# Kernel optimization log

Hardware: AMD Instinct MI355X
Metric: run time of the kernel (lower is better)

## Reference

```python
import jax, jax.numpy as jnp
from jax import lax
import numpy as np

B, S, T = 1024, 512, 48


def setup_inputs() -> dict:
    key = jax.random.key(0)
    k1, k2, k3, k4, k5, k6 = jax.random.split(key, 6)
    emissions = jax.random.normal(k1, (B, S, T), dtype=jnp.float32)
    tags = jax.random.randint(k2, (B, S), 0, T, dtype=jnp.int32)
    # variable-length mask; length >= 1 so position 0 is always valid
    lengths = jax.random.randint(k3, (B,), 1, S + 1, dtype=jnp.int32)
    mask = (jnp.arange(S)[None, :] < lengths[:, None]).astype(jnp.float32)
    transitions = jax.random.normal(k4, (T, T), dtype=jnp.float32)
    start_transitions = jax.random.normal(k5, (T,), dtype=jnp.float32)
    end_transitions = jax.random.normal(k6, (T,), dtype=jnp.float32)
    return {
        "emissions": emissions,
        "tags": tags,
        "mask": mask,
        "transitions": transitions,
        "start_transitions": start_transitions,
        "end_transitions": end_transitions,
    }


def _gold_score(emissions, tags, mask, transitions, start_transitions, end_transitions):
    # score of the gold tag sequence (vectorized over time)
    score = start_transitions[tags[:, 0]]
    score = score + jnp.take_along_axis(emissions[:, 0], tags[:, 0:1], axis=1)[:, 0]
    # NOTE: original code indexes transitions[cur_tag, prev_tag] here (faithful)
    trans_sc = transitions[tags[:, 1:], tags[:, :-1]]                      # [B, S-1]
    emit_sc = jnp.take_along_axis(emissions[:, 1:], tags[:, 1:, None], axis=2)[..., 0]
    score = score + jnp.sum((trans_sc + emit_sc) * mask[:, 1:], axis=1)
    seq_last = mask.sum(axis=1).astype(jnp.int32) - 1                      # [B]
    last_tags = jnp.take_along_axis(tags, seq_last[:, None], axis=1)[:, 0]
    return score + end_transitions[last_tags]


def _forward_algorithm(emissions, mask, transitions, start_transitions, end_transitions):
    # log-partition via logsumexp recurrence, lax.scan over time
    init = start_transitions[None, :] + emissions[:, 0]                    # [B, T]

    def step(score, xs):
        em_i, m_i = xs                                                     # [B,T], [B]
        # next[b, cur] = logsumexp_prev(score[b,prev] + trans[prev,cur] + em[b,cur])
        ns = jax.nn.logsumexp(score[:, :, None] + transitions[None] + em_i[:, None, :], axis=1)
        score = jnp.where(m_i[:, None] > 0, ns, score)
        return score, None

    xs = (jnp.swapaxes(emissions[:, 1:], 0, 1), jnp.swapaxes(mask[:, 1:], 0, 1))
    score, _ = lax.scan(step, init, xs)
    return jax.nn.logsumexp(score + end_transitions[None, :], axis=1)      # [B]


def reference(emissions, tags, mask, transitions, start_transitions, end_transitions):
    gold = _gold_score(emissions, tags, mask, transitions, start_transitions, end_transitions)
    fwd = _forward_algorithm(emissions, mask, transitions, start_transitions, end_transitions)
    return (fwd - gold).mean()
```

## Files before the change

kernel.cpp:

```cpp
#include <hip/hip_runtime.h>


#define T 48
#define SLEN 512
#define BATCH 1024

typedef _Float16 h2 __attribute__((ext_vector_type(2)));

__device__ __forceinline__ float wave_sum(float v) {
#pragma unroll
    for (int m = 32; m >= 1; m >>= 1) v += __shfl_xor(v, m, 64);
    return v;
}
__device__ __forceinline__ float wave_max(float v) {
#pragma unroll
    for (int m = 32; m >= 1; m >>= 1) v = fmaxf(v, __shfl_xor(v, m, 64));
    return v;
}
__device__ __forceinline__ float rlane(float v, int k) {
    return __int_as_float(__builtin_amdgcn_readlane(__float_as_int(v), k));
}
__device__ __forceinline__ float fdot2(h2 a, h2 b, float c) {
#if __has_builtin(__builtin_amdgcn_fdot2)
    return __builtin_amdgcn_fdot2(a, b, c, false);
#else
    return fmaf((float)a[1], (float)b[1], fmaf((float)a[0], (float)b[0], c));
#endif
}

#define QH(S, k) (__builtin_bit_cast(h2, (S)[k]))

#define DOTS48(S, E, A0, A1, A2, A3)                 \
    _Pragma("unroll")                                \
    for (int t = 0; t < 24; t += 4) {                \
        A0 = fdot2(QH(S, t + 0), E[t + 0], A0);      \
        A1 = fdot2(QH(S, t + 1), E[t + 1], A1);      \
        A2 = fdot2(QH(S, t + 2), E[t + 2], A2);      \
        A3 = fdot2(QH(S, t + 3), E[t + 3], A3);      \
    }

#define BCAST24(DST, VAL)                                                 \
    {                                                                     \
        unsigned hp_ = (unsigned)__builtin_bit_cast(unsigned short,       \
                          (_Float16)(VAL));                               \
        unsigned op_ = __shfl_xor(hp_, 1, 64);                            \
        unsigned lo_ = (lane & 1) ? op_ : hp_;                            \
        unsigned hi_ = (lane & 1) ? hp_ : op_;                            \
        unsigned pk_ = lo_ | (hi_ << 16);                                 \
        _Pragma("unroll")                                                 \
        for (int k = 0; k < 24; ++k)                                      \
            (DST)[k] = (unsigned)__builtin_amdgcn_readlane((int)pk_,      \
                                                            2 * k);       \
    }

__global__ __launch_bounds__(64) void crf_kernel(
    const float* __restrict__ em,
    const int*   __restrict__ tags,
    const float* __restrict__ mask,
    const float* __restrict__ trans,
    const float* __restrict__ start_t,
    const float* __restrict__ end_t,
    float*       __restrict__ out)
{
    constexpr float LOG2E = 1.4426950408889634f;
    constexpr float LN2   = 0.6931471805599453f;
    constexpr float ESC   = -8.0f;

    const int b    = blockIdx.x;
    const int lane = threadIdx.x;
    const int j    = lane < T ? lane : (T - 1);

    const float* em_b   = em   + (size_t)b * SLEN * T;
    const float* mask_b = mask + (size_t)b * SLEN;
    const int*   tags_b = tags + (size_t)b * SLEN;

    float msum = 0.f;
    for (int s = lane; s < SLEN; s += 64) msum += mask_b[s];
    msum = wave_sum(msum);
    const int len = (int)(msum + 0.5f);
    const int nb  = (len - 1) >> 1;
    const int nf  = (len - 1) - nb;

    float g = 0.f;
    for (int i = lane; i < len; i += 64) {
        if (i >= 1) {
            const int tc = tags_b[i];
            const int tp = tags_b[i - 1];
            g += trans[tc * T + tp] + em_b[(size_t)i * T + tc];
        }
    }
    g = wave_sum(g);

    h2 Ec[24], Er[24];
#pragma unroll
    for (int k = 0; k < T; k += 2) {
        h2 c, r;
        c[0] = (_Float16)exp2f(trans[(k    ) * T + j] * LOG2E + ESC);
        c[1] = (_Float16)exp2f(trans[(k + 1) * T + j] * LOG2E + ESC);
        r[0] = (_Float16)exp2f(trans[j * T + (k    )] * LOG2E + ESC);
        r[1] = (_Float16)exp2f(trans[j * T + (k + 1)] * LOG2E + ESC);
        Ec[k >> 1] = c; Er[k >> 1] = r;
    }

    const float z0 = (start_t[j] + em_b[j]) * LOG2E;
    const float m0 = wave_max(z0);
    float pf = exp2f(z0 - m0);
    float u  = exp2f(end_t[j] * LOG2E);
    float Lf = m0, Lb = 0.f;

    const float* ep = em_b + j;
    const int maxoff = (SLEN - 1) * T;

    const float vlast  = ep[(size_t)(len - 1) * T];
    const float vextra = ep[(size_t)nf * T];

    unsigned sf[24], sb[24];
    BCAST24(sf, pf)
    BCAST24(sb, fminf(u * exp2f(vlast * LOG2E), 60000.f))

    int fo = T;
    float f0 = ep[fo < maxoff ? fo : maxoff]; fo += T;
    float f1 = ep[fo < maxoff ? fo : maxoff]; fo += T;
    float f2 = ep[fo < maxoff ? fo : maxoff]; fo += T;
    float f3 = ep[fo < maxoff ? fo : maxoff]; fo += T;
    int bo = (len - 2) * T;
    float e0 = ep[bo > 0 ? bo : 0]; bo -= T;
    float e1 = ep[bo > 0 ? bo : 0]; bo -= T;
    float e2 = ep[bo > 0 ? bo : 0]; bo -= T;
    float e3 = ep[bo > 0 ? bo : 0]; bo -= T;

    auto rescale = [&](float& v, float& L) {
        float m = fmaxf(fmaxf(rlane(v, 0), rlane(v, 16)),
                        fmaxf(rlane(v, 32), rlane(v, 47)));
        int e = ((__float_as_int(m) >> 23) & 255) - 127;
        e = e < -64 ? -64 : e;
        v *= __int_as_float((127 - e) << 23);
        L += (float)e;
    };

    auto jiter = [&](float& fe, float& be, bool resc) {
        float wf = exp2f(fe * LOG2E);
        fe = ep[fo < maxoff ? fo : maxoff]; fo += T;
        float a0=0.f, a1=0.f, a2=0.f, a3=0.f;
        DOTS48(sf, Ec, a0, a1, a2, a3)
        float pn = ((a0 + a1) + (a2 + a3)) * wf;
        if (resc) rescale(pn, Lf);
        pf = pn;
        BCAST24(sf, fminf(pn, 60000.f))
        float wb = exp2f(be * LOG2E);
        be = ep[bo > 0 ? bo : 0]; bo -= T;
        float c0=0.f, c1=0.f, c2=0.f, c3=0.f;
        DOTS48(sb, Er, c0, c1, c2, c3)
        float un = (c0 + c1) + (c2 + c3);
        if (resc) rescale(un, Lb);
        u = un;
        BCAST24(sb, fminf(un * wb, 60000.f))
    };

    int rem = nb;
    while (rem >= 4) {
        jiter(f0, e0, false);
        jiter(f1, e1, false);
        jiter(f2, e2, false);
        jiter(f3, e3, true);
        rem -= 4;
    }
    if (rem > 0) { jiter(f0, e0, false);
        if (rem > 1) { jiter(f1, e1, false);
            if (rem > 2) jiter(f2, e2, false); } }

    if (nf > nb) {
        float wf = exp2f(vextra * LOG2E);
        float a0=0.f, a1=0.f, a2=0.f, a3=0.f;
        DOTS48(sf, Ec, a0, a1, a2, a3)
        pf = ((a0 + a1) + (a2 + a3)) * wf;
    }

    Lf += 8.0f * (float)nf;
    Lb += 8.0f * (float)nb;
    const float v  = (lane < T) ? pf * u : 0.f;
    const float S_ = wave_sum(v);
    const float fwd = (Lf + Lb + log2f(S_)) * LN2;

    if (lane == 0) {
        const int t0 = tags_b[0];
        const int tl = tags_b[len - 1];
        const float gold = g + start_t[t0] + em_b[t0] + end_t[tl];
        atomicAdd(out, (fwd - gold) * (1.0f / (float)BATCH));
    }
}

extern "C" void kernel_launch(void* const* d_in, const int* in_sizes, int n_in,
                              void* d_out, int out_size, void* d_ws, size_t ws_size,
                              hipStream_t stream) {
    const float* em      = (const float*)d_in[0];
    const int*   tags    = (const int*)  d_in[1];
    const float* mask    = (const float*)d_in[2];
    const float* trans   = (const float*)d_in[3];
    const float* start_t = (const float*)d_in[4];
    const float* end_t   = (const float*)d_in[5];
    float* out = (float*)d_out;

    hipMemsetAsync(out, 0, sizeof(float), stream);
    crf_kernel<<<BATCH, 64, 0, stream>>>(em, tags, mask, trans, start_t, end_t, out);
}
```

Measured before the change: 231.1 us.

## Split forward and backward recurrences across two waves per block

Instead of one wave interleaving the forward and backward half-recurrences, each block now runs two waves: wave 0 runs the forward alpha chain and wave 1 runs the backward beta chain, each with a single transition table in registers. The two halves are combined through shared memory after a barrier. This is meant to shorten the serial per-wave dependency chain and cut register pressure, since each wave holds 24 packed transition values instead of 48. The cost is twice as many waves competing for SIMD issue slots. The interleaving within one wave previously gave some ILP that is now lost.

```diff
diff --git a/kernel.cpp b/kernel.cpp
--- a/kernel.cpp
+++ b/kernel.cpp
@@ -53,7 +53,7 @@
                                                             2 * k);       \
     }
 
-__global__ __launch_bounds__(64) void crf_kernel(
+__global__ __launch_bounds__(128) void crf_kernel(
     const float* __restrict__ em,
     const int*   __restrict__ tags,
     const float* __restrict__ mask,
@@ -67,7 +67,9 @@
     constexpr float ESC   = -8.0f;
 
     const int b    = blockIdx.x;
-    const int lane = threadIdx.x;
+    const int tid  = threadIdx.x;
+    const int w    = tid >> 6;
+    const int lane = tid & 63;
     const int j    = lane < T ? lane : (T - 1);
 
     const float* em_b   = em   + (size_t)b * SLEN * T;
@@ -80,56 +82,61 @@
     const int len = (int)(msum + 0.5f);
     const int nb  = (len - 1) >> 1;
     const int nf  = (len - 1) - nb;
-
-    float g = 0.f;
-    for (int i = lane; i < len; i += 64) {
-        if (i >= 1) {
-            const int tc = tags_b[i];
-            const int tp = tags_b[i - 1];
-            g += trans[tc * T + tp] + em_b[(size_t)i * T + tc];
-        }
-    }
-    g = wave_sum(g);
-
-    h2 Ec[24], Er[24];
+    const int steps = w ? nb : nf;
+
+    h2 E[24];
 #pragma unroll
     for (int k = 0; k < T; k += 2) {
-        h2 c, r;
-        c[0] = (_Float16)exp2f(trans[(k    ) * T + j] * LOG2E + ESC);
-        c[1] = (_Float16)exp2f(trans[(k + 1) * T + j] * LOG2E + ESC);
-        r[0] = (_Float16)exp2f(trans[j * T + (k    )] * LOG2E + ESC);
-        r[1] = (_Float16)exp2f(trans[j * T + (k + 1)] * LOG2E + ESC);
-        Ec[k >> 1] = c; Er[k >> 1] = r;
-    }
-
-    const float z0 = (start_t[j] + em_b[j]) * LOG2E;
-    const float m0 = wave_max(z0);
-    float pf = exp2f(z0 - m0);
-    float u  = exp2f(end_t[j] * LOG2E);
-    float Lf = m0, Lb = 0.f;
+        const int i0 = w ? (j * T + k)     : (k * T + j);
+        const int i1 = w ? (j * T + k + 1) : ((k + 1) * T + j);
+        h2 e;
+        e[0] = (_Float16)exp2f(trans[i0] * LOG2E + ESC);
+        e[1] = (_Float16)exp2f(trans[i1] * LOG2E + ESC);
+        E[k >> 1] = e;
+    }
 
     const float* ep = em_b + j;
     const int maxoff = (SLEN - 1) * T;
 
-    const float vlast  = ep[(size_t)(len - 1) * T];
-    const float vextra = ep[(size_t)nf * T];
-
-    unsigned sf[24], sb[24];
-    BCAST24(sf, pf)
-    BCAST24(sb, fminf(u * exp2f(vlast * LOG2E), 60000.f))
-
-    int fo = T;
-    float f0 = ep[fo < maxoff ? fo : maxoff]; fo += T;
-    float f1 = ep[fo < maxoff ? fo : maxoff]; fo += T;
-    float f2 = ep[fo < maxoff ? fo : maxoff]; fo += T;
-    float f3 = ep[fo < maxoff ? fo : maxoff]; fo += T;
-    int bo = (len - 2) * T;
-    float e0 = ep[bo > 0 ? bo : 0]; bo -= T;
-    float e1 = ep[bo > 0 ? bo : 0]; bo -= T;
-    float e2 = ep[bo > 0 ? bo : 0]; bo -= T;
-    float e3 = ep[bo > 0 ? bo : 0]; bo -= T;
-
-    auto rescale = [&](float& v, float& L) {
+    float st, L, pubinit;
+    if (w == 0) {
+        const float z0 = (start_t[j] + em_b[j]) * LOG2E;
+        const float m0 = wave_max(z0);
+        st = exp2f(z0 - m0); L = m0;
+        pubinit = st;
+    } else {
+        st = exp2f(end_t[j] * LOG2E); L = 0.f;
+        const float vlast = ep[(size_t)(len - 1) * T];
+        pubinit = fminf(st * exp2f(vlast * LOG2E), 60000.f);
+    }
+    unsigned sf[24];
+    BCAST24(sf, pubinit)
+
+    float g = 0.f;
+    if (w == 0) {
+        for (int i = lane; i < len; i += 64) {
+            if (i >= 1) {
+                const int tc = tags_b[i];
+                const int tp = tags_b[i - 1];
+                g += trans[tc * T + tp] + em_b[(size_t)i * T + tc];
+            }
+        }
+        g = wave_sum(g);
+    }
+
+    const int dlt = w ? -T : T;
+    int off = w ? (len - 2) * T : T;
+    auto ldem = [&]() -> float {
+        int oc = off;
+        oc = oc < 0 ? 0 : oc;
+        oc = oc > maxoff ? maxoff : oc;
+        const float r = ep[oc];
+        off += dlt;
+        return r;
+    };
+    float f0 = ldem(), f1 = ldem(), f2 = ldem(), f3 = ldem();
+
+    auto rescale = [&](float& v) {
         float m = fmaxf(fmaxf(rlane(v, 0), rlane(v, 16)),
                         fmaxf(rlane(v, 32), rlane(v, 47)));
         int e = ((__float_as_int(m) >> 23) & 255) - 127;
@@ -138,55 +145,47 @@
         L += (float)e;
     };
 
-    auto jiter = [&](float& fe, float& be, bool resc) {
-        float wf = exp2f(fe * LOG2E);
-        fe = ep[fo < maxoff ? fo : maxoff]; fo += T;
-        float a0=0.f, a1=0.f, a2=0.f, a3=0.f;
-        DOTS48(sf, Ec, a0, a1, a2, a3)
-        float pn = ((a0 + a1) + (a2 + a3)) * wf;
-        if (resc) rescale(pn, Lf);
-        pf = pn;
-        BCAST24(sf, fminf(pn, 60000.f))
-        float wb = exp2f(be * LOG2E);
-        be = ep[bo > 0 ? bo : 0]; bo -= T;
-        float c0=0.f, c1=0.f, c2=0.f, c3=0.f;
-        DOTS48(sb, Er, c0, c1, c2, c3)
-        float un = (c0 + c1) + (c2 + c3);
-        if (resc) rescale(un, Lb);
-        u = un;
-        BCAST24(sb, fminf(un * wb, 60000.f))
+    auto step = [&](float& fe, bool resc) {
+        const float wv = exp2f(fe * LOG2E);
+        fe = ldem();
+        float a0 = 0.f, a1 = 0.f, a2 = 0.f, a3 = 0.f;
+        DOTS48(sf, E, a0, a1, a2, a3)
+        float s = (a0 + a1) + (a2 + a3);
+        if (w == 0) s *= wv;
+        if (resc) rescale(s);
+        st = s;
+        const float pub = fminf(w ? s * wv : s, 60000.f);
+        BCAST24(sf, pub)
     };
 
-    int rem = nb;
+    int rem = steps;
     while (rem >= 4) {
-        jiter(f0, e0, false);
-        jiter(f1, e1, false);
-        jiter(f2, e2, false);
-        jiter(f3, e3, true);
+        step(f0, false); step(f1, false); step(f2, false); step(f3, true);
         rem -= 4;
     }
-    if (rem > 0) { jiter(f0, e0, false);
-        if (rem > 1) { jiter(f1, e1, false);
-            if (rem > 2) jiter(f2, e2, false); } }
-
-    if (nf > nb) {
-        float wf = exp2f(vextra * LOG2E);
-        float a0=0.f, a1=0.f, a2=0.f, a3=0.f;
-        DOTS48(sf, Ec, a0, a1, a2, a3)
-        pf = ((a0 + a1) + (a2 + a3)) * wf;
-    }
-
-    Lf += 8.0f * (float)nf;
-    Lb += 8.0f * (float)nb;
-    const float v  = (lane < T) ? pf * u : 0.f;
-    const float S_ = wave_sum(v);
-    const float fwd = (Lf + Lb + log2f(S_)) * LN2;
-
-    if (lane == 0) {
-        const int t0 = tags_b[0];
-        const int tl = tags_b[len - 1];
-        const float gold = g + start_t[t0] + em_b[t0] + end_t[tl];
-        atomicAdd(out, (fwd - gold) * (1.0f / (float)BATCH));
+    if (rem > 0) { step(f0, false);
+        if (rem > 1) { step(f1, false);
+            if (rem > 2) step(f2, false); } }
+
+    __shared__ float shu[T];
+    __shared__ float shL[2];
+    if (w == 0) {
+        if (lane == 0) shL[0] = L + 8.0f * (float)nf;
+    } else {
+        if (lane < T) shu[lane] = st;
+        if (lane == 0) shL[1] = L + 8.0f * (float)nb;
+    }
+    __syncthreads();
+    if (w == 0) {
+        const float v  = (lane < T) ? st * shu[lane] : 0.f;
+        const float S_ = wave_sum(v);
+        const float fwd = (shL[0] + shL[1] + log2f(S_)) * LN2;
+        if (lane == 0) {
+            const int t0 = tags_b[0];
+            const int tl = tags_b[len - 1];
+            const float gold = g + start_t[t0] + em_b[t0] + end_t[tl];
+            atomicAdd(out, (fwd - gold) * (1.0f / (float)BATCH));
+        }
     }
 }
 
@@ -202,5 +201,5 @@
     float* out = (float*)d_out;
 
     hipMemsetAsync(out, 0, sizeof(float), stream);
-    crf_kernel<<<BATCH, 64, 0, stream>>>(em, tags, mask, trans, start_t, end_t, out);
-}
+    crf_kernel<<<BATCH, 128, 0, stream>>>(em, tags, mask, trans, start_t, end_t, out);
+}
```

New measurement: 222.6 us. 3.7% less time.
